# Optimization experiments

Measured on AMD Instinct MI355X. Metric: run time of the kernel, lower is better.

Reference implementation:

```python
import jax, jax.numpy as jnp
import numpy as np

N_NODES = 200000
N_EDGES = 500000
N_RELS = 256
D = 256  # rnn_in_dim == rnn_hid_dim


def setup_inputs() -> dict:
    key = jax.random.key(0)
    ks = jax.random.split(key, 8)
    src_nid = jax.random.randint(ks[0], (N_EDGES,), 0, N_NODES, dtype=jnp.int32)
    dst_nid = jax.random.randint(ks[1], (N_EDGES,), 0, N_NODES, dtype=jnp.int32)
    rel = jax.random.randint(ks[2], (N_EDGES,), 0, N_RELS, dtype=jnp.int32)
    static_entity_emb = jax.random.normal(ks[3], (N_NODES, D), dtype=jnp.float32)
    dynamic_relation_emb = jax.random.normal(ks[4], (N_RELS, 1, D, 2), dtype=jnp.float32)
    s = 1.0 / np.sqrt(D)
    W_ih = jax.random.uniform(ks[5], (3 * D, D), jnp.float32, -s, s)
    W_hh = jax.random.uniform(ks[6], (3 * D, D), jnp.float32, -s, s)
    kb1, kb2 = jax.random.split(ks[7])
    b_ih = jax.random.uniform(kb1, (3 * D,), jnp.float32, -s, s)
    b_hh = jax.random.uniform(kb2, (3 * D,), jnp.float32, -s, s)
    return {"src_nid": src_nid, "dst_nid": dst_nid, "rel": rel,
            "static_entity_emb": static_entity_emb,
            "dynamic_relation_emb": dynamic_relation_emb,
            "W_ih": W_ih, "W_hh": W_hh, "b_ih": b_ih, "b_hh": b_hh}


def _segment_mean(x, ids, num_segments):
    # x: [E, D], ids: [E] -> [R, D] mean per relation (0 where empty, as scatter_mean)
    sums = jax.ops.segment_sum(x, ids, num_segments=num_segments)
    cnts = jax.ops.segment_sum(jnp.ones((ids.shape[0],), x.dtype), ids,
                               num_segments=num_segments)
    return sums / jnp.maximum(cnts, 1.0)[:, None]


def _gru_cell(x, h, W_ih, W_hh, b_ih, b_hh):
    # PyTorch GRU cell, single step. x,h: [R, H]
    gi = x @ W_ih.T + b_ih            # [R, 3H]
    gh = h @ W_hh.T + b_hh            # [R, 3H]
    i_r, i_z, i_n = jnp.split(gi, 3, axis=-1)
    h_r, h_z, h_n = jnp.split(gh, 3, axis=-1)
    r = jax.nn.sigmoid(i_r + h_r)
    z = jax.nn.sigmoid(i_z + h_z)
    n = jnp.tanh(i_n + r * h_n)
    return (1.0 - z) * n + z * h


def reference(src_nid, dst_nid, rel, static_entity_emb, dynamic_relation_emb,
              W_ih, W_hh, b_ih, b_hh):
    R = dynamic_relation_emb.shape[0]
    # gather node embeddings by edge endpoints, mean-reduce per relation
    src_avg = _segment_mean(static_entity_emb[src_nid], rel, R)  # [R, D]
    dst_avg = _segment_mean(static_entity_emb[dst_nid], rel, R)  # [R, D]
    h_src = dynamic_relation_emb[:, 0, :, 0]  # num_layers==1 -> [R, H]
    h_dst = dynamic_relation_emb[:, 0, :, 1]
    new_src = _gru_cell(src_avg, h_src, W_ih, W_hh, b_ih, b_hh)
    new_dst = _gru_cell(dst_avg, h_dst, W_ih, W_hh, b_ih, b_hh)
    # [R, num_layers=1, H, 2]
    return jnp.stack([new_src, new_dst], axis=-1)[:, None, :, :]
```

## Files before the change

### kernel.cpp

```cpp
#include <hip/hip_runtime.h>
#include <math.h>

#define D 256
#define R 256
#define DIMC 64

__device__ __forceinline__ float sigmoidf(float x) {
    return 1.0f / (1.0f + expf(-x));
}

__global__ void zero_ws(float* ws, int n) {
    int i = blockIdx.x * blockDim.x + threadIdx.x;
    if (i < n) ws[i] = 0.0f;
}

__global__ __launch_bounds__(256) void hist_kernel(const int* __restrict__ rel,
                                                   int E,
                                                   float* __restrict__ counts) {
    __shared__ int h[R];
    h[threadIdx.x] = 0;
    __syncthreads();
    for (int e = blockIdx.x * blockDim.x + threadIdx.x; e < E;
         e += gridDim.x * blockDim.x)
        atomicAdd(&h[rel[e]], 1);
    __syncthreads();
    atomicAdd(&counts[threadIdx.x], (float)h[threadIdx.x]);
}

__global__ __launch_bounds__(1024, 8) void scatter_kernel(
    const int* __restrict__ src_nid, const int* __restrict__ dst_nid,
    const int* __restrict__ rel, const float* __restrict__ emb,
    float* __restrict__ src_sum, float* __restrict__ dst_sum, int E, int epb) {
    __shared__ float acc[R * DIMC];
    const int tid = threadIdx.x;
    for (int i = tid; i < R * DIMC; i += 1024) acc[i] = 0.0f;
    __syncthreads();

    const int* nids = blockIdx.z ? dst_nid : src_nid;
    float* gsum     = blockIdx.z ? dst_sum : src_sum;
    const int dimbase = blockIdx.y * DIMC;
    const int lane = tid & 63;
    const int wave = tid >> 6;
    const int start = blockIdx.x * epb;
    const int end   = (start + epb < E) ? (start + epb) : E;

    for (int base = start + wave * 64; base < end; base += 1024) {
        const int e = base + lane;
        const bool valid = e < end;
        int mynid = 0, myrel = 0;
        if (valid) {
            mynid = nids[e];
            myrel = rel[e];
        }
        const float4* row =
            (const float4*)(emb + (size_t)mynid * D + dimbase);
#pragma unroll
        for (int c = 0; c < 4; c++) {
            float4 v[4];
#pragma unroll
            for (int k = 0; k < 4; k++) v[k] = row[c * 4 + k];
            if (valid) {
#pragma unroll
                for (int k = 0; k < 4; k++) {
                    const int d0 = c * 16 + k * 4;
                    atomicAdd(&acc[(d0 + 0) * R + (myrel ^ ((d0 + 0) & 31))], v[k].x);
                    atomicAdd(&acc[(d0 + 1) * R + (myrel ^ ((d0 + 1) & 31))], v[k].y);
                    atomicAdd(&acc[(d0 + 2) * R + (myrel ^ ((d0 + 2) & 31))], v[k].z);
                    atomicAdd(&acc[(d0 + 3) * R + (myrel ^ ((d0 + 3) & 31))], v[k].w);
                }
            }
        }
    }
    __syncthreads();
    for (int i = tid; i < R * DIMC; i += 1024) {
        const int d = i & (DIMC - 1);
        const int r = i >> 6;
        atomicAdd(&gsum[r * D + dimbase + d], acc[d * R + (r ^ (d & 31))]);
    }
}

__global__ __launch_bounds__(512) void gru_kernel(
    const float* __restrict__ src_sum, const float* __restrict__ dst_sum,
    const float* __restrict__ counts, const float* __restrict__ dyn,
    const float* __restrict__ W_ih, const float* __restrict__ W_hh,
    const float* __restrict__ b_ih, const float* __restrict__ b_hh,
    float* __restrict__ out) {
    __shared__ float x2[2][D], h2[2][D];
    const int r = blockIdx.x, t = threadIdx.x;
    const int s = t >> 8;
    const int tt = t & 255;
    const float inv = 1.0f / fmaxf(counts[r], 1.0f);
    float h_old;
    if (s == 0) {
        x2[0][tt] = src_sum[r * D + tt] * inv;
        h_old = dyn[(r * D + tt) * 2 + 0];
        h2[0][tt] = h_old;
    } else {
        x2[1][tt] = dst_sum[r * D + tt] * inv;
        h_old = dyn[(r * D + tt) * 2 + 1];
        h2[1][tt] = h_old;
    }
    __syncthreads();
    const float* xs = x2[s];
    const float* hs = h2[s];

    float gi[3], gh[3];
#pragma unroll
    for (int g = 0; g < 3; g++) {
        const int row = g * D + tt;
        const float4* wi = (const float4*)(W_ih + (size_t)row * D);
        const float4* wh = (const float4*)(W_hh + (size_t)row * D);
        float ai = 0.f, ah = 0.f;
        for (int k = 0; k < D / 4; k++) {
            float4 a = wi[k];
            float4 b = wh[k];
            int k4 = k * 4;
            ai += a.x * xs[k4] + a.y * xs[k4 + 1] + a.z * xs[k4 + 2] + a.w * xs[k4 + 3];
            ah += b.x * hs[k4] + b.y * hs[k4 + 1] + b.z * hs[k4 + 2] + b.w * hs[k4 + 3];
        }
        gi[g] = ai + b_ih[row];
        gh[g] = ah + b_hh[row];
    }
    const float rr = sigmoidf(gi[0] + gh[0]);
    const float zz = sigmoidf(gi[1] + gh[1]);
    const float nn = tanhf(gi[2] + rr * gh[2]);
    const float nh = (1.0f - zz) * nn + zz * h_old;

    out[(r * D + tt) * 2 + s] = nh;
}

extern "C" void kernel_launch(void* const* d_in, const int* in_sizes, int n_in,
                              void* d_out, int out_size, void* d_ws, size_t ws_size,
                              hipStream_t stream) {
    const int* src_nid = (const int*)d_in[0];
    const int* dst_nid = (const int*)d_in[1];
    const int* rel     = (const int*)d_in[2];
    const float* emb   = (const float*)d_in[3];
    const float* dyn   = (const float*)d_in[4];
    const float* W_ih  = (const float*)d_in[5];
    const float* W_hh  = (const float*)d_in[6];
    const float* b_ih  = (const float*)d_in[7];
    const float* b_hh  = (const float*)d_in[8];
    float* out = (float*)d_out;
    const int E = in_sizes[0];

    float* ws      = (float*)d_ws;
    float* src_sum = ws;
    float* dst_sum = ws + R * D;
    float* counts  = ws + 2 * R * D;
    const int nzero = 2 * R * D + R;

    zero_ws<<<(nzero + 255) / 256, 256, 0, stream>>>(ws, nzero);
    hist_kernel<<<256, 256, 0, stream>>>(rel, E, counts);

    const int chunks = 64;
    const int epb = (E + chunks - 1) / chunks;
    scatter_kernel<<<dim3(chunks, 4, 2), 1024, 0, stream>>>(
        src_nid, dst_nid, rel, emb, src_sum, dst_sum, E, epb);

    gru_kernel<<<R, 512, 0, stream>>>(src_sum, dst_sum, counts, dyn, W_ih, W_hh,
                                      b_ih, b_hh, out);
}
```

Measured before the change: 1.596 ms.

## Bin edges by node-id range so each XCD gathers a cache-local embedding slice

Adds a counting-sort pass that buckets edges by source/destination node id into 64 ranges, packing node id and relation into one word. The gather kernel maps blocks so each XCD handles a contiguous set of buckets, which is meant to keep that slice of the embedding table resident in the XCD-local L2 and cut random HBM traffic. The cost is extra histogram, prefix and binning kernels with global atomics, plus workspace for the bins. The original scatter path stays as a fallback when the workspace is too small.

```diff
diff --git a/kernel.cpp b/kernel.cpp
--- a/kernel.cpp
+++ b/kernel.cpp
@@ -4,6 +4,9 @@
 #define D 256
 #define R 256
 #define DIMC 64
+#define NNODES 200000
+#define NB 64
+#define BUCKET ((NNODES + NB - 1) / NB)
 
 __device__ __forceinline__ float sigmoidf(float x) {
     return 1.0f / (1.0f + expf(-x));
@@ -12,6 +15,116 @@
 __global__ void zero_ws(float* ws, int n) {
     int i = blockIdx.x * blockDim.x + threadIdx.x;
     if (i < n) ws[i] = 0.0f;
+}
+
+__global__ __launch_bounds__(256) void hist2_kernel(
+    const int* __restrict__ rel, const int* __restrict__ src_nid,
+    const int* __restrict__ dst_nid, int E, float* __restrict__ counts,
+    int* __restrict__ bcnt) {
+    __shared__ int h[R];
+    __shared__ int hb[2 * NB];
+    const int t = threadIdx.x;
+    h[t] = 0;
+    if (t < 2 * NB) hb[t] = 0;
+    __syncthreads();
+    for (int e = blockIdx.x * 256 + t; e < E; e += gridDim.x * 256) {
+        atomicAdd(&h[rel[e]], 1);
+        atomicAdd(&hb[src_nid[e] / BUCKET], 1);
+        atomicAdd(&hb[NB + dst_nid[e] / BUCKET], 1);
+    }
+    __syncthreads();
+    atomicAdd(&counts[t], (float)h[t]);
+    if (t < 2 * NB) atomicAdd(&bcnt[t], hb[t]);
+}
+
+__global__ void prefix_kernel(const int* __restrict__ bcnt, int* __restrict__ off,
+                              int* __restrict__ cur) {
+    __shared__ int c[2 * NB];
+    const int t = threadIdx.x;
+    if (t < 2 * NB) c[t] = bcnt[t];
+    __syncthreads();
+    if (t == 0) {
+        int a = 0;
+        for (int b = 0; b < NB; b++) { off[b] = a; cur[b * 64] = a; a += c[b]; }
+        off[NB] = a;
+        a = 0;
+        for (int b = 0; b < NB; b++) {
+            off[NB + 1 + b] = a;
+            cur[(NB + b) * 64] = a;
+            a += c[NB + b];
+        }
+        off[2 * NB + 1] = a;
+    }
+}
+
+__global__ __launch_bounds__(256) void bin_kernel(
+    const int* __restrict__ src_nid, const int* __restrict__ dst_nid,
+    const int* __restrict__ rel, int E, int* __restrict__ cur,
+    unsigned* __restrict__ bin0, unsigned* __restrict__ bin1) {
+    for (int e = blockIdx.x * 256 + threadIdx.x; e < E; e += gridDim.x * 256) {
+        const unsigned rl = (unsigned)rel[e];
+        const int n0 = src_nid[e];
+        const int p0 = atomicAdd(&cur[(n0 / BUCKET) * 64], 1);
+        bin0[p0] = (unsigned)n0 | (rl << 18);
+        const int n1 = dst_nid[e];
+        const int p1 = atomicAdd(&cur[(NB + n1 / BUCKET) * 64], 1);
+        bin1[p1] = (unsigned)n1 | (rl << 18);
+    }
+}
+
+__global__ __launch_bounds__(1024, 8) void gather_kernel(
+    const unsigned* __restrict__ bin0, const unsigned* __restrict__ bin1,
+    const int* __restrict__ off, const float* __restrict__ emb,
+    float* __restrict__ src_sum, float* __restrict__ dst_sum) {
+    __shared__ float acc[R * DIMC];
+    const int tid = threadIdx.x;
+    for (int i = tid; i < R * DIMC; i += 1024) acc[i] = 0.0f;
+    __syncthreads();
+
+    const int g = blockIdx.x;
+    const int xcd = g & 7;
+    const int lid = g >> 3;
+    const int sl = lid & 7;
+    const int y = (lid >> 3) & 3;
+    const int z = lid >> 5;
+    const unsigned* bin = z ? bin1 : bin0;
+    const int* offs = off + z * (NB + 1);
+    float* gsum = z ? dst_sum : src_sum;
+    const int dimbase = y * DIMC;
+
+    for (int p = 0; p < NB / 8; p++) {
+        const int b = xcd * (NB / 8) + p;
+        const int lo = offs[b], hi = offs[b + 1];
+        const int cnt = hi - lo;
+        const int c0 = lo + ((cnt * sl) >> 3);
+        const int c1 = lo + ((cnt * (sl + 1)) >> 3);
+        for (int idx = c0 + tid; idx < c1; idx += 1024) {
+            const unsigned key = bin[idx];
+            const int nid = (int)(key & 0x3FFFFu);
+            const int rl = (int)(key >> 18);
+            const float4* row = (const float4*)(emb + (size_t)nid * D + dimbase);
+#pragma unroll
+            for (int c = 0; c < 4; c++) {
+                float4 v[4];
+#pragma unroll
+                for (int k = 0; k < 4; k++) v[k] = row[c * 4 + k];
+#pragma unroll
+                for (int k = 0; k < 4; k++) {
+                    const int d0 = c * 16 + k * 4;
+                    atomicAdd(&acc[(d0 + 0) * R + (rl ^ ((d0 + 0) & 31))], v[k].x);
+                    atomicAdd(&acc[(d0 + 1) * R + (rl ^ ((d0 + 1) & 31))], v[k].y);
+                    atomicAdd(&acc[(d0 + 2) * R + (rl ^ ((d0 + 2) & 31))], v[k].z);
+                    atomicAdd(&acc[(d0 + 3) * R + (rl ^ ((d0 + 3) & 31))], v[k].w);
+                }
+            }
+        }
+    }
+    __syncthreads();
+    for (int i = tid; i < R * DIMC; i += 1024) {
+        const int d = i & (DIMC - 1);
+        const int r = i >> 6;
+        atomicAdd(&gsum[r * D + dimbase + d], acc[d * R + (r ^ (d & 31))]);
+    }
 }
 
 __global__ __launch_bounds__(256) void hist_kernel(const int* __restrict__ rel,
@@ -27,7 +140,7 @@
     atomicAdd(&counts[threadIdx.x], (float)h[threadIdx.x]);
 }
 
-__global__ __launch_bounds__(1024, 8) void scatter_kernel(
+__global__ __launch_bounds__(1024, 8) void scatter_fallback(
     const int* __restrict__ src_nid, const int* __restrict__ dst_nid,
     const int* __restrict__ rel, const float* __restrict__ emb,
     float* __restrict__ src_sum, float* __restrict__ dst_sum, int E, int epb) {
@@ -35,25 +148,19 @@
     const int tid = threadIdx.x;
     for (int i = tid; i < R * DIMC; i += 1024) acc[i] = 0.0f;
     __syncthreads();
-
     const int* nids = blockIdx.z ? dst_nid : src_nid;
-    float* gsum     = blockIdx.z ? dst_sum : src_sum;
+    float* gsum = blockIdx.z ? dst_sum : src_sum;
     const int dimbase = blockIdx.y * DIMC;
     const int lane = tid & 63;
     const int wave = tid >> 6;
     const int start = blockIdx.x * epb;
-    const int end   = (start + epb < E) ? (start + epb) : E;
-
+    const int end = (start + epb < E) ? (start + epb) : E;
     for (int base = start + wave * 64; base < end; base += 1024) {
         const int e = base + lane;
         const bool valid = e < end;
         int mynid = 0, myrel = 0;
-        if (valid) {
-            mynid = nids[e];
-            myrel = rel[e];
-        }
-        const float4* row =
-            (const float4*)(emb + (size_t)mynid * D + dimbase);
+        if (valid) { mynid = nids[e]; myrel = rel[e]; }
+        const float4* row = (const float4*)(emb + (size_t)mynid * D + dimbase);
 #pragma unroll
         for (int c = 0; c < 4; c++) {
             float4 v[4];
@@ -125,7 +232,6 @@
     const float zz = sigmoidf(gi[1] + gh[1]);
     const float nn = tanhf(gi[2] + rr * gh[2]);
     const float nh = (1.0f - zz) * nn + zz * h_old;
-
     out[(r * D + tt) * 2 + s] = nh;
 }
 
@@ -148,15 +254,29 @@
     float* src_sum = ws;
     float* dst_sum = ws + R * D;
     float* counts  = ws + 2 * R * D;
-    const int nzero = 2 * R * D + R;
-
-    zero_ws<<<(nzero + 255) / 256, 256, 0, stream>>>(ws, nzero);
-    hist_kernel<<<256, 256, 0, stream>>>(rel, E, counts);
-
-    const int chunks = 64;
-    const int epb = (E + chunks - 1) / chunks;
-    scatter_kernel<<<dim3(chunks, 4, 2), 1024, 0, stream>>>(
-        src_nid, dst_nid, rel, emb, src_sum, dst_sum, E, epb);
+    int*   bcnt    = (int*)(counts + R);
+    int*   off     = bcnt + 2 * NB;
+    int*   cur     = off + 2 * NB + 2;
+    unsigned* bin0 = (unsigned*)(cur + 128 * 64);
+    unsigned* bin1 = bin0 + E;
+    const size_t needed = (size_t)((char*)(bin1 + E) - (char*)ws);
+
+    if (ws_size >= needed) {
+        const int nzero = 2 * R * D + R + 2 * NB;
+        zero_ws<<<(nzero + 255) / 256, 256, 0, stream>>>(ws, nzero);
+        hist2_kernel<<<256, 256, 0, stream>>>(rel, src_nid, dst_nid, E, counts, bcnt);
+        prefix_kernel<<<1, 128, 0, stream>>>(bcnt, off, cur);
+        bin_kernel<<<512, 256, 0, stream>>>(src_nid, dst_nid, rel, E, cur, bin0, bin1);
+        gather_kernel<<<512, 1024, 0, stream>>>(bin0, bin1, off, emb, src_sum, dst_sum);
+    } else {
+        const int nzero = 2 * R * D + R;
+        zero_ws<<<(nzero + 255) / 256, 256, 0, stream>>>(ws, nzero);
+        hist_kernel<<<256, 256, 0, stream>>>(rel, E, counts);
+        const int chunks = 64;
+        const int epb = (E + chunks - 1) / chunks;
+        scatter_fallback<<<dim3(chunks, 4, 2), 1024, 0, stream>>>(
+            src_nid, dst_nid, rel, emb, src_sum, dst_sum, E, epb);
+    }
 
     gru_kernel<<<R, 512, 0, stream>>>(src_sum, dst_sum, counts, dyn, W_ih, W_hh,
                                       b_ih, b_hh, out);
```

Measured after the change: 1.743 ms. +9.2%, slower.
